# Optimization experiments

Hardware: AMD Instinct MI355X
Metric: run time of the kernel (lower is better)

The kernel has to match this reference:

```python
import jax, jax.numpy as jnp
import numpy as np

# ---- static config (matches init_kwargs) ----
B, S, E = 1, 2048, 2048
H, G, D = 32, 8, 64            # query heads, kv groups, head_dim
GS = H // G                    # group size = 4
SW = 128                       # sliding window
LAYER_IDX = 0                  # even -> sliding-window mask active
ROPE_BASE = 10000.0
ORIG_CTX = 4096.0              # yarn_original_context_length
YARN_SCALE = 2.0               # yarn_scaling_factor
BETA_FAST, BETA_SLOW = 32.0, 1.0


def _rope_sincos(position_ids):
    # YaRN-adjusted RoPE angles, computed directly at position_ids.
    freqs = 1.0 / ROPE_BASE ** (jnp.arange(0, D, 2, dtype=jnp.float32) / D)  # [D/2]
    wave_len = 2.0 * jnp.pi / freqs
    low = ORIG_CTX / BETA_FAST
    high = ORIG_CTX / BETA_SLOW
    t = jnp.clip((wave_len - low) / (high - low), 0.0, 1.0)
    eff = freqs * (1.0 - t) + (freqs / YARN_SCALE) * t
    conc = 0.1 * jnp.log(jnp.float32(YARN_SCALE)) + 1.0
    ang = position_ids[..., None].astype(jnp.float32) * eff * conc           # [B,S,D/2]
    ang = jnp.concatenate([ang, ang], axis=-1)                               # [B,S,D]
    # add head axis for broadcast over [B,H,S,D]
    return jnp.sin(ang)[:, None], jnp.cos(ang)[:, None]


def _apply_rope(x, sin, cos):
    x1, x2 = x[..., : D // 2], x[..., D // 2 :]
    rotated = jnp.concatenate([-x2, x1], axis=-1)
    return x * cos + rotated * sin


def setup_inputs() -> dict:
    key = jax.random.key(0)
    ks = jax.random.split(key, 6)
    x = jax.random.normal(ks[0], (B, S, E), dtype=jnp.float32)
    position_ids = jnp.broadcast_to(jnp.arange(S, dtype=jnp.int32), (B, S))
    # additive causal mask: -inf above the diagonal
    i = jnp.arange(S)[:, None]
    j = jnp.arange(S)[None, :]
    attn_mask = jnp.where(j > i, -jnp.inf, 0.0).astype(jnp.float32)[None, None]  # [1,1,S,S]
    sc = 0.02
    Wqkv = jax.random.normal(ks[1], ((H + 2 * G) * D, E), dtype=jnp.float32) * sc
    bqkv = jax.random.normal(ks[2], ((H + 2 * G) * D,), dtype=jnp.float32) * sc
    Wout = jax.random.normal(ks[3], (E, H * D), dtype=jnp.float32) * sc
    bout = jax.random.normal(ks[4], (E,), dtype=jnp.float32) * sc
    sinks = jax.random.normal(ks[5], (1, H, 1, 1), dtype=jnp.float32)
    return {"x": x, "position_ids": position_ids, "attn_mask": attn_mask,
            "Wqkv": Wqkv, "bqkv": bqkv, "Wout": Wout, "bout": bout, "sinks": sinks}


def reference(x, position_ids, attn_mask, Wqkv, bqkv, Wout, bout, sinks):
    b, s, _ = x.shape
    qkv = (x @ Wqkv.T + bqkv).reshape(b, s, H + 2 * G, D)
    Q = qkv[:, :, :H].transpose(0, 2, 1, 3)              # [B,H,S,D]
    K = qkv[:, :, H : H + G].transpose(0, 2, 1, 3)       # [B,G,S,D]
    V = qkv[:, :, H + G :].transpose(0, 2, 1, 3)         # [B,G,S,D]

    sin, cos = _rope_sincos(position_ids)
    Q = _apply_rope(Q, sin, cos)
    K = _apply_rope(K, sin, cos)

    # GQA: group query heads, no K/V duplication
    Qg = Q.reshape(b, G, GS, s, D)
    scores = jnp.einsum("bgmqd,bgkd->bgmqk", Qg, K) / (D ** 0.5)  # [B,G,GS,S,S]
    scores = scores.reshape(b, H, s, s) + attn_mask

    # sliding-window mask (layer_idx even, kv_len > sliding_window)
    if LAYER_IDX % 2 == 0 and s > SW:
        i = jnp.arange(s)[:, None]
        j = jnp.arange(s)[None, :]
        scores = jnp.where(j <= i - SW, -jnp.inf, scores)

    # learned sink logit prepended before softmax, then dropped
    sink = jnp.broadcast_to(sinks, (b, H, s, 1))
    attn = jax.nn.softmax(jnp.concatenate([sink, scores], axis=-1), axis=-1)[..., 1:]

    ctx = jnp.einsum("bgmqk,bgkd->bgmqd", attn.reshape(b, G, GS, s, s), V)
    ctx = ctx.reshape(b, H, s, D).transpose(0, 2, 1, 3).reshape(b, s, H * D)
    return ctx @ Wout.T + bout
```

## Files before the change

kernel.cpp:

```cpp
#include <hip/hip_runtime.h>
#include <cstdint>

#define S_LEN 2048
#define EMB   2048
#define NHEAD 32
#define NKV   8
#define HDIM  64
#define NQKV  3072

typedef __attribute__((ext_vector_type(8))) short bf16x8;
typedef __attribute__((ext_vector_type(4))) float f32x4;

__device__ __forceinline__ unsigned short f2bf(float f){
  union { float f; unsigned int u; } v; v.f = f;
  unsigned int r = v.u + 0x7FFFu + ((v.u >> 16) & 1u);
  return (unsigned short)(r >> 16);
}
__device__ __forceinline__ float bf2f(unsigned short u){
  union { unsigned int u; float f; } v; v.u = ((unsigned int)u) << 16;
  return v.f;
}

__global__ __launch_bounds__(256) void cvt3_kernel(const float* __restrict__ a, unsigned short* __restrict__ da, int na,
                                                   const float* __restrict__ b, unsigned short* __restrict__ db, int nb,
                                                   const float* __restrict__ c, unsigned short* __restrict__ dc, int nc){
  int i = blockIdx.x * 256 + threadIdx.x;
  const float* s; unsigned short* d;
  if (i < na){ s = a; d = da; }
  else if (i < na + nb){ s = b; d = db; i -= na; }
  else if (i < na + nb + nc){ s = c; d = dc; i -= na + nb; }
  else return;
  const float4 v = ((const float4*)s)[i];
  ushort4 o;
  o.x = f2bf(v.x); o.y = f2bf(v.y); o.z = f2bf(v.z); o.w = f2bf(v.w);
  ((ushort4*)d)[i] = o;
}

template<int OUT_BF16, int ROPE>
__global__ __launch_bounds__(256) void gemm_bt(const unsigned short* __restrict__ A,
                                               const unsigned short* __restrict__ B,
                                               const float* __restrict__ bias,
                                               void* __restrict__ Cout,
                                               const int* __restrict__ pos,
                                               int M, int N, int K){
  __shared__ unsigned short As[64*32];
  __shared__ unsigned short Bs[128*32];
  const int tid  = threadIdx.x;
  const int lane = tid & 63;
  const int wid  = tid >> 6;
  const int m0 = blockIdx.y * 64;
  const int n0 = blockIdx.x * 128;
  const int wm = (wid >> 1) * 32;
  const int wn = (wid & 1) * 64;
  const int fm = lane & 15;
  const int q8 = (lane >> 4) * 8;
  const int quad = lane >> 4;

  f32x4 acc[2][4];
#pragma unroll
  for (int i = 0; i < 2; ++i)
#pragma unroll
    for (int j = 0; j < 4; ++j) acc[i][j] = {0.f, 0.f, 0.f, 0.f};

  const int srow = lane >> 2;
  const int scol = (lane & 3) * 8;
  const unsigned short* Ag = A + (size_t)(m0 + wid*16 + srow) * K + scol;
  const unsigned short* Bg = B + (size_t)(n0 + wid*32 + srow) * K + scol;
  unsigned short* AsW = &As[(wid*16)*32];
  unsigned short* BsW = &Bs[(wid*32)*32];

  for (int k0 = 0; k0 < K; k0 += 32){
    __syncthreads();
    __builtin_amdgcn_global_load_lds((const __attribute__((address_space(1))) void*)(Ag + k0),
        (__attribute__((address_space(3))) void*)AsW, 16, 0, 0);
    __builtin_amdgcn_global_load_lds((const __attribute__((address_space(1))) void*)(Bg + k0),
        (__attribute__((address_space(3))) void*)BsW, 16, 0, 0);
    __builtin_amdgcn_global_load_lds((const __attribute__((address_space(1))) void*)(Bg + k0 + (size_t)16*K),
        (__attribute__((address_space(3))) void*)(BsW + 16*32), 16, 0, 0);
    __syncthreads();

    bf16x8 af[2], bfr[4];
#pragma unroll
    for (int i = 0; i < 2; ++i) af[i]  = *(const bf16x8*)&As[(wm + i*16 + fm)*32 + q8];
#pragma unroll
    for (int j = 0; j < 4; ++j) bfr[j] = *(const bf16x8*)&Bs[(wn + j*16 + fm)*32 + q8];
#pragma unroll
    for (int i = 0; i < 2; ++i)
#pragma unroll
      for (int j = 0; j < 4; ++j)
        acc[i][j] = __builtin_amdgcn_mfma_f32_16x16x32_bf16(af[i], bfr[j], acc[i][j], 0, 0, 0);
  }

  float v[2][4][4];
#pragma unroll
  for (int j = 0; j < 4; ++j){
    const float bv = bias[n0 + wn + j*16 + fm];
#pragma unroll
    for (int i = 0; i < 2; ++i)
#pragma unroll
      for (int r = 0; r < 4; ++r) v[i][j][r] = acc[i][j][r] + bv;
  }

  if (ROPE && (n0 + wn) < 2560){
    float cc[2][4][2], ss[2][4][2];
#pragma unroll
    for (int jp = 0; jp < 2; ++jp){
      const float ifr = (float)(jp*16 + fm);
      const float freq = __expf(-ifr * (9.210340371976184f / 32.0f));
      const float wl = 6.283185307179586f / freq;
      float t = fminf(fmaxf((wl - 128.0f) * (1.0f / 3968.0f), 0.f), 1.f);
      const float eff = freq * (1.0f - 0.5f * t) * 1.0693147180559945f;
#pragma unroll
      for (int i = 0; i < 2; ++i)
#pragma unroll
        for (int r = 0; r < 4; ++r){
          const int row = m0 + wm + i*16 + quad*4 + r;
          const float ang = (float)pos[row] * eff;
          __sincosf(ang, &ss[i][r][jp], &cc[i][r][jp]);
        }
    }
    float o[2][4][4];
#pragma unroll
    for (int i = 0; i < 2; ++i)
#pragma unroll
      for (int j = 0; j < 4; ++j){
        const int jp = j & 1;
        const float sgn = (j < 2) ? -1.f : 1.f;
#pragma unroll
        for (int r = 0; r < 4; ++r)
          o[i][j][r] = v[i][j][r]*cc[i][r][jp] + sgn*v[i][j^2][r]*ss[i][r][jp];
      }
#pragma unroll
    for (int i = 0; i < 2; ++i)
#pragma unroll
      for (int j = 0; j < 4; ++j)
#pragma unroll
        for (int r = 0; r < 4; ++r) v[i][j][r] = o[i][j][r];
  }

#pragma unroll
  for (int j = 0; j < 4; ++j){
    const int col = n0 + wn + j*16 + fm;
#pragma unroll
    for (int i = 0; i < 2; ++i){
#pragma unroll
      for (int r = 0; r < 4; ++r){
        const int row = m0 + wm + i*16 + quad*4 + r;
        if (OUT_BF16) ((unsigned short*)Cout)[(size_t)row*N + col] = f2bf(v[i][j][r]);
        else          ((float*)Cout)[(size_t)row*N + col] = v[i][j][r];
      }
    }
  }
}

__global__ __launch_bounds__(256) void attn_kernel(const unsigned short* __restrict__ qkv,
                                                   const float* __restrict__ sinks,
                                                   unsigned short* __restrict__ ctxb){
  const int h  = blockIdx.y;
  const int q0 = blockIdx.x * 64;
  const int g  = h >> 2;
  const int tid  = threadIdx.x;
  const int lane = tid & 63;
  const int wid  = tid >> 6;
  const int fm   = lane & 15;
  const int quad = lane >> 4;

  __shared__ unsigned short Ks[2*64*40];
  __shared__ unsigned short Vt[2*64*34];
  __shared__ unsigned short Pl[4*2*16*40];

  const int qrow = q0 + wid*16 + fm;
  bf16x8 aq[2];
#pragma unroll
  for (int ks = 0; ks < 2; ++ks)
    aq[ks] = *(const bf16x8*)(qkv + (size_t)qrow*NQKV + h*HDIM + ks*32 + quad*8);

  f32x4 o[4];
#pragma unroll
  for (int nt = 0; nt < 4; ++nt) o[nt] = {0.f, 0.f, 0.f, 0.f};
  float m_[4], l_[4];
#pragma unroll
  for (int r = 0; r < 4; ++r){ m_[r] = -30000.f; l_[r] = 0.f; }

  const int qbase = q0 + wid*16 + quad*4;
  int cs0 = q0 - 128; if (cs0 < 0) cs0 = 0;
  unsigned short* plw = &Pl[wid*1280];

  for (int cs = cs0; cs <= q0; cs += 64){
    __syncthreads();
#pragma unroll
    for (int it = 0; it < 2; ++it){
      const int e = (tid + it*256) * 8;
      const int key = e >> 6, d0 = e & 63;
      const unsigned short* kp = qkv + (size_t)(cs + key)*NQKV + EMB + g*HDIM + d0;
      *(bf16x8*)&Ks[(d0>>5)*2560 + key*40 + (d0 & 31)] = *(const bf16x8*)kp;
      const bf16x8 vv = *(const bf16x8*)(kp + NKV*HDIM);
      const unsigned short* vs = (const unsigned short*)&vv;
      unsigned short* vt = &Vt[(key>>5)*2176 + (key & 31)];
#pragma unroll
      for (int j = 0; j < 8; ++j) vt[(d0 + j)*34] = vs[j];
    }
    __syncthreads();

    f32x4 sa[4];
#pragma unroll
    for (int nt = 0; nt < 4; ++nt){
      sa[nt] = {0.f, 0.f, 0.f, 0.f};
#pragma unroll
      for (int ks = 0; ks < 2; ++ks){
        const bf16x8 bk = *(const bf16x8*)&Ks[ks*2560 + (nt*16 + fm)*40 + quad*8];
        sa[nt] = __builtin_amdgcn_mfma_f32_16x16x32_bf16(aq[ks], bk, sa[nt], 0, 0, 0);
      }
    }

#pragma unroll
    for (int nt = 0; nt < 4; ++nt){
      const int key = cs + nt*16 + fm;
#pragma unroll
      for (int r = 0; r < 4; ++r){
        const float s = sa[nt][r] * 0.125f;
        const bool ok = (unsigned)(qbase + r - key) < 128u;
        sa[nt][r] = ok ? s : -1e30f;
      }
    }

#pragma unroll
    for (int r = 0; r < 4; ++r){
      float t = fmaxf(fmaxf(sa[0][r], sa[1][r]), fmaxf(sa[2][r], sa[3][r]));
#pragma unroll
      for (int off = 1; off < 16; off <<= 1) t = fmaxf(t, __shfl_xor(t, off, 64));
      const float nm = fmaxf(m_[r], t);
      const float al = __expf(m_[r] - nm);
#pragma unroll
      for (int nt = 0; nt < 4; ++nt) sa[nt][r] = __expf(sa[nt][r] - nm);
      float ts = (sa[0][r] + sa[1][r]) + (sa[2][r] + sa[3][r]);
#pragma unroll
      for (int off = 1; off < 16; off <<= 1) ts += __shfl_xor(ts, off, 64);
      l_[r] = l_[r]*al + ts;
      m_[r] = nm;
#pragma unroll
      for (int nt = 0; nt < 4; ++nt) o[nt][r] *= al;
    }

#pragma unroll
    for (int nt = 0; nt < 4; ++nt)
#pragma unroll
      for (int r = 0; r < 4; ++r)
        plw[(nt>>1)*640 + (quad*4 + r)*40 + (nt&1)*16 + fm] = f2bf(sa[nt][r]);
    __asm__ volatile("s_waitcnt lgkmcnt(0)" ::: "memory");

    bf16x8 pa[2];
#pragma unroll
    for (int ks = 0; ks < 2; ++ks)
      pa[ks] = *(const bf16x8*)&plw[ks*640 + fm*40 + quad*8];
    const unsigned int* vb = (const unsigned int*)Vt;
#pragma unroll
    for (int nt = 0; nt < 4; ++nt){
#pragma unroll
      for (int ks = 0; ks < 2; ++ks){
        const int ui = ks*1088 + (nt*16 + fm)*17 + quad*4;
        union { unsigned int u[4]; bf16x8 v; } bb;
        bb.u[0] = vb[ui+0]; bb.u[1] = vb[ui+1]; bb.u[2] = vb[ui+2]; bb.u[3] = vb[ui+3];
        o[nt] = __builtin_amdgcn_mfma_f32_16x16x32_bf16(pa[ks], bb.v, o[nt], 0, 0, 0);
      }
    }
  }

  const float snk = sinks[h];
#pragma unroll
  for (int r = 0; r < 4; ++r){
    const float nm = fmaxf(m_[r], snk);
    const float e  = __expf(m_[r] - nm);
    const float denom = l_[r]*e + __expf(snk - nm);
    const float sc = e / denom;
    const size_t row = (size_t)(qbase + r)*EMB + h*HDIM;
#pragma unroll
    for (int nt = 0; nt < 4; ++nt)
      ctxb[row + nt*16 + fm] = f2bf(o[nt][r] * sc);
  }
}

extern "C" void kernel_launch(void* const* d_in, const int* in_sizes, int n_in,
                              void* d_out, int out_size, void* d_ws, size_t ws_size,
                              hipStream_t stream){
  const float* x     = (const float*)d_in[0];
  const int*   pos   = (const int*)  d_in[1];
  const float* Wqkv  = (const float*)d_in[3];
  const float* bqkv  = (const float*)d_in[4];
  const float* Wout  = (const float*)d_in[5];
  const float* bout  = (const float*)d_in[6];
  const float* sinks = (const float*)d_in[7];

  char* ws = (char*)d_ws;
  unsigned short* xb   = (unsigned short*)(ws);
  unsigned short* wqb  = (unsigned short*)(ws + 8388608);
  unsigned short* wob  = (unsigned short*)(ws + 20971520);
  unsigned short* qkv  = (unsigned short*)(ws + 29360128);
  unsigned short* ctxb = (unsigned short*)(ws + 41943040);

  cvt3_kernel<<<dim3(14336), dim3(256), 0, stream>>>(x, xb, 1048576,
                                                     Wqkv, wqb, 1572864,
                                                     Wout, wob, 1048576);

  gemm_bt<1,1><<<dim3(24, 32), dim3(256), 0, stream>>>(xb, wqb, bqkv, (void*)qkv, pos, 2048, 3072, 2048);
  attn_kernel<<<dim3(32, 32), dim3(256), 0, stream>>>(qkv, sinks, ctxb);
  gemm_bt<0,0><<<dim3(16, 32), dim3(256), 0, stream>>>(ctxb, wob, bout, d_out, nullptr, 2048, 2048, 2048);
}
```

Baseline: 214.5 us.

## Triple-buffer GEMM LDS tiles with async global_load_lds prefetch two stages ahead

Replaces the single-buffered GEMM main loop, which had two barriers per K step, with a 3-stage LDS ring. Loads for step k+2 are issued while step k computes, and fine-grained vmcnt waits plus a single s_barrier per iteration replace the full syncthreads pair. The goal is to hide global-memory latency behind the MFMA work. In exchange LDS use triples, which may lower occupancy, and correctness now depends on the hand-written vmcnt counts.

Measured after the change: 214.9 us. About the same (+0.2%).

```diff
diff --git a/kernel.cpp b/kernel.cpp
--- a/kernel.cpp
+++ b/kernel.cpp
@@ -10,6 +10,9 @@
 
 typedef __attribute__((ext_vector_type(8))) short bf16x8;
 typedef __attribute__((ext_vector_type(4))) float f32x4;
+
+#define GPTR const __attribute__((address_space(1))) void*
+#define LPTR __attribute__((address_space(3))) void*
 
 __device__ __forceinline__ unsigned short f2bf(float f){
   union { float f; unsigned int u; } v; v.f = f;
@@ -43,8 +46,8 @@
                                                void* __restrict__ Cout,
                                                const int* __restrict__ pos,
                                                int M, int N, int K){
-  __shared__ unsigned short As[64*32];
-  __shared__ unsigned short Bs[128*32];
+  __shared__ unsigned short As[3*64*32];
+  __shared__ unsigned short Bs[3*128*32];
   const int tid  = threadIdx.x;
   const int lane = tid & 63;
   const int wid  = tid >> 6;
@@ -69,26 +72,40 @@
   unsigned short* AsW = &As[(wid*16)*32];
   unsigned short* BsW = &Bs[(wid*32)*32];
 
-  for (int k0 = 0; k0 < K; k0 += 32){
-    __syncthreads();
-    __builtin_amdgcn_global_load_lds((const __attribute__((address_space(1))) void*)(Ag + k0),
-        (__attribute__((address_space(3))) void*)AsW, 16, 0, 0);
-    __builtin_amdgcn_global_load_lds((const __attribute__((address_space(1))) void*)(Bg + k0),
-        (__attribute__((address_space(3))) void*)BsW, 16, 0, 0);
-    __builtin_amdgcn_global_load_lds((const __attribute__((address_space(1))) void*)(Bg + k0 + (size_t)16*K),
-        (__attribute__((address_space(3))) void*)(BsW + 16*32), 16, 0, 0);
-    __syncthreads();
-
+  auto stage = [&](int k0, int buf){
+    unsigned short* dA = AsW + buf*(64*32);
+    unsigned short* dB = BsW + buf*(128*32);
+    __builtin_amdgcn_global_load_lds((GPTR)(Ag + k0), (LPTR)dA, 16, 0, 0);
+    __builtin_amdgcn_global_load_lds((GPTR)(Bg + k0), (LPTR)dB, 16, 0, 0);
+    __builtin_amdgcn_global_load_lds((GPTR)(Bg + k0 + (size_t)16*K), (LPTR)(dB + 16*32), 16, 0, 0);
+  };
+
+  stage(0, 0);
+  stage(32, 1);
+
+  const int KITER = K >> 5;
+  int bcur = 0;
+  for (int it = 0; it < KITER; ++it){
+    if (it + 1 < KITER) asm volatile("s_waitcnt vmcnt(3)" ::: "memory");
+    else                asm volatile("s_waitcnt vmcnt(0)" ::: "memory");
+    asm volatile("s_barrier" ::: "memory");
+    if (it + 2 < KITER){
+      int bnext = bcur + 2; if (bnext >= 3) bnext -= 3;
+      stage((it + 2) * 32, bnext);
+    }
+    const unsigned short* Ab = As + bcur*(64*32);
+    const unsigned short* Bb = Bs + bcur*(128*32);
     bf16x8 af[2], bfr[4];
 #pragma unroll
-    for (int i = 0; i < 2; ++i) af[i]  = *(const bf16x8*)&As[(wm + i*16 + fm)*32 + q8];
-#pragma unroll
-    for (int j = 0; j < 4; ++j) bfr[j] = *(const bf16x8*)&Bs[(wn + j*16 + fm)*32 + q8];
+    for (int i = 0; i < 2; ++i) af[i]  = *(const bf16x8*)&Ab[(wm + i*16 + fm)*32 + q8];
+#pragma unroll
+    for (int j = 0; j < 4; ++j) bfr[j] = *(const bf16x8*)&Bb[(wn + j*16 + fm)*32 + q8];
 #pragma unroll
     for (int i = 0; i < 2; ++i)
 #pragma unroll
       for (int j = 0; j < 4; ++j)
         acc[i][j] = __builtin_amdgcn_mfma_f32_16x16x32_bf16(af[i], bfr[j], acc[i][j], 0, 0, 0);
+    bcur = (bcur == 2) ? 0 : bcur + 1;
   }
 
   float v[2][4][4];
```
